# Kernel tuning notes

Measured on AMD Instinct MI355X. Metric: run time of the kernel, lower is better.

The kernel has to match this reference:

```python
import jax, jax.numpy as jnp
import numpy as np

U = 512  # units

def hard_sigmoid(x):
    # Keras hard_sigmoid: clip(0.2*x + 0.5, 0, 1)
    return jnp.clip(0.2 * x + 0.5, 0.0, 1.0)

def setup_inputs() -> dict:
    key = jax.random.key(0)
    ks = jax.random.split(key, 9)
    B, T, A, D = 64, 2048, 512, 512  # batch, annotation steps, annotation units, input dim
    s = lambda k, shape, scale: jax.random.normal(k, shape, jnp.float32) * scale
    return {
        "inputs": s(ks[0], (B, D), 1.0),
        "h": s(ks[1], (B, U), 1.0),
        "c": s(ks[2], (B, U), 1.0),
        "annotations": s(ks[3], (B, T, A), 1.0),
        "kernel": s(ks[4], (D + A, 4 * U), 0.02),
        "recurrent_kernel": s(ks[5], (U, 4 * U), 0.02),
        "bias": jnp.zeros((6 * U,), jnp.float32).at[U:2 * U].set(1.0),  # unit_forget_bias
        "kernel_u": s(ks[6], (A, U), 0.02),
        "kernel_w": s(ks[7], (U, U), 0.02),
        "kernel_v": s(ks[8], (U,), 0.02),
    }

def reference(inputs, h, c, annotations, kernel, recurrent_kernel, bias, kernel_u, kernel_w, kernel_v):
    bias_u = bias[4 * U:5 * U]
    # precomputed annotation projection (done once in build()): [B,T,U]
    uh = jnp.einsum('bta,au->btu', annotations, kernel_u) + bias_u
    # Bahdanau attention scores
    Wxstm = h @ kernel_w                                   # [B,U]
    et = jnp.einsum('btu,u->bt', jnp.tanh(uh + Wxstm[:, None, :]), kernel_v)
    at = jax.nn.softmax(et, axis=1)                        # exp/sum in source == softmax
    context = jnp.einsum('bt,bta->ba', at, annotations)    # [B,A]
    x = jnp.concatenate([inputs, context], axis=-1)        # [B, D+A]
    z = x @ kernel + h @ recurrent_kernel + bias[:4 * U]   # [B,4U]
    i = hard_sigmoid(z[:, :U])
    f = hard_sigmoid(z[:, U:2 * U])
    c_new = f * c + i * jnp.tanh(z[:, 2 * U:3 * U])
    o = hard_sigmoid(z[:, 3 * U:])
    h_new = o * jnp.tanh(c_new)
    return h_new
```

## Files before the change

kernel.cpp:

```cpp
#include <hip/hip_runtime.h>

constexpr int U = 512;
constexpr int B = 64;
constexpr int T = 2048;
constexpr int A = 512;

typedef __attribute__((ext_vector_type(8))) short short8;
typedef __attribute__((ext_vector_type(4))) float f32x4;

__device__ __forceinline__ unsigned short f32_to_bf16(float f) {
    unsigned int b = __float_as_uint(f);
    unsigned int r = (b + 0x7FFFu + ((b >> 16) & 1u)) >> 16;
    return (unsigned short)r;
}

__device__ __forceinline__ float fast_tanh(float x) {
    float e = exp2f(x * 2.885390081777927f);
    return (e - 1.0f) * __builtin_amdgcn_rcpf(e + 1.0f);
}

__device__ __forceinline__ float hard_sigmoid(float z) {
    return fminf(fmaxf(0.2f * z + 0.5f, 0.0f), 1.0f);
}

__global__ __launch_bounds__(256) void k_prep_s(const float* __restrict__ h,
                                                const float* __restrict__ kw,
                                                float* __restrict__ Sp) {
    int b = blockIdx.x >> 2;
    int kc = blockIdx.x & 3;
    int u = threadIdx.x;
    const float* hb = h + b * U + kc * 128;
    const float* kwb = kw + (size_t)kc * 128 * U;
    float a0 = 0.f, a1 = 0.f;
#pragma unroll 4
    for (int k = 0; k < 128; ++k) {
        float hv = hb[k];
        a0 += hv * kwb[(size_t)k * U + u];
        a1 += hv * kwb[(size_t)k * U + u + 256];
    }
    float* p = Sp + ((size_t)kc * 64 + b) * U;
    p[u] = a0;
    p[u + 256] = a1;
}

__global__ __launch_bounds__(256) void k_s_reduce(const float* __restrict__ Sp,
                                                  const float* __restrict__ bias,
                                                  float* __restrict__ S) {
    int gid = blockIdx.x * 256 + threadIdx.x;
    int b = gid >> 9, u = gid & 511;
    float s = bias[4 * U + u];
#pragma unroll
    for (int kc = 0; kc < 4; ++kc) s += Sp[((size_t)kc * 64 + b) * U + u];
    S[gid] = s;
}

__global__ __launch_bounds__(256) void k_prep_kut(const float* __restrict__ ku,
                                                  unsigned short* __restrict__ kut) {
    __shared__ float tile[32][33];
    int a0 = (blockIdx.x >> 4) << 5;
    int u0 = (blockIdx.x & 15) << 5;
    int c = threadIdx.x & 31, r0 = threadIdx.x >> 5;
#pragma unroll
    for (int p = 0; p < 4; ++p) {
        int r = r0 + p * 8;
        tile[r][c] = ku[(a0 + r) * U + u0 + c];
    }
    __syncthreads();
#pragma unroll
    for (int p = 0; p < 4; ++p) {
        int r = r0 + p * 8;
        kut[(u0 + r) * A + a0 + c] = f32_to_bf16(tile[c][r]);
    }
}

__global__ __launch_bounds__(256) void k_prep_wt(const float* __restrict__ kern,
                                                 const float* __restrict__ rk,
                                                 unsigned short* __restrict__ Wt) {
    __shared__ float tile[32][33];
    int k0 = blockIdx.x << 5;
    int j0 = blockIdx.y << 5;
    int c = threadIdx.x & 31, r0 = threadIdx.x >> 5;
#pragma unroll
    for (int p = 0; p < 4; ++p) {
        int r = r0 + p * 8;
        int k = k0 + r;
        float val = (k < 1024) ? kern[k * 2048 + j0 + c]
                               : rk[(k - 1024) * 2048 + j0 + c];
        tile[r][c] = val;
    }
    __syncthreads();
#pragma unroll
    for (int p = 0; p < 4; ++p) {
        int r = r0 + p * 8;
        Wt[(size_t)(j0 + r) * 1536 + k0 + c] = f32_to_bf16(tile[c][r]);
    }
}

__global__ __launch_bounds__(256) void k_gemm_et(const float* __restrict__ ann,
                                                 const unsigned short* __restrict__ kut,
                                                 const float* __restrict__ S,
                                                 const float* __restrict__ v,
                                                 float* __restrict__ etp) {
    __shared__ unsigned short As[128 * 88];
    __shared__ unsigned short Bs[128 * 64];
    __shared__ float red[4][64];

    const int tid = threadIdx.x;
    const int wave = tid >> 6;
    const int lane = tid & 63;
    const int lanelo = lane & 15;
    const int quad = lane >> 4;
    const int wm = wave >> 1, wn = wave & 1;

    const int mt = blockIdx.x >> 2;
    const int nt = blockIdx.x & 3;
    const int b = mt >> 4;
    const float* aBase = ann + (size_t)mt * 128 * A;
    const unsigned short* bBase = kut + (size_t)nt * 128 * A;

    f32x4 acc[4][4];
#pragma unroll
    for (int i = 0; i < 4; ++i)
#pragma unroll
        for (int j = 0; j < 4; ++j) acc[i][j] = {0.f, 0.f, 0.f, 0.f};

    for (int k0 = 0; k0 < A; k0 += 64) {
#pragma unroll
        for (int p = 0; p < 4; ++p) {
            int flat = p * 4096 + wave * 1024 + lane * 16;
            int nl = flat >> 7;
            int d = ((flat >> 4) & 7) ^ (nl & 7);
            __builtin_amdgcn_global_load_lds(
                (const __attribute__((address_space(1))) void*)(bBase + (size_t)nl * A + k0 + d * 8),
                (__attribute__((address_space(3))) void*)((char*)Bs + p * 4096 + wave * 1024),
                16, 0, 0);
        }
#pragma unroll
        for (int p = 0; p < 4; ++p) {
            int flat8 = p * 256 + tid;
            int row = flat8 >> 3;
            int c8 = flat8 & 7;
            const float* src = aBase + (size_t)row * A + k0 + c8 * 8;
            f32x4 v0 = *(const f32x4*)src;
            f32x4 v1 = *(const f32x4*)(src + 4);
            short8 pk;
            pk[0] = (short)f32_to_bf16(v0.x);
            pk[1] = (short)f32_to_bf16(v0.y);
            pk[2] = (short)f32_to_bf16(v0.z);
            pk[3] = (short)f32_to_bf16(v0.w);
            pk[4] = (short)f32_to_bf16(v1.x);
            pk[5] = (short)f32_to_bf16(v1.y);
            pk[6] = (short)f32_to_bf16(v1.z);
            pk[7] = (short)f32_to_bf16(v1.w);
            *(short8*)&As[row * 88 + c8 * 8] = pk;
        }
        __syncthreads();
#pragma unroll
        for (int s = 0; s < 2; ++s) {
            short8 af[4], bfr[4];
#pragma unroll
            for (int mi = 0; mi < 4; ++mi) {
                int row = wm * 64 + mi * 16 + lanelo;
                af[mi] = *(const short8*)&As[row * 88 + s * 32 + quad * 8];
            }
#pragma unroll
            for (int ni = 0; ni < 4; ++ni) {
                int nl = wn * 64 + ni * 16 + lanelo;
                int ch = (s * 4 + quad) ^ (nl & 7);
                bfr[ni] = *(const short8*)&Bs[nl * 64 + ch * 8];
            }
#pragma unroll
            for (int mi = 0; mi < 4; ++mi)
#pragma unroll
                for (int ni = 0; ni < 4; ++ni)
                    acc[mi][ni] = __builtin_amdgcn_mfma_f32_16x16x32_bf16(
                        af[mi], bfr[ni], acc[mi][ni], 0, 0, 0);
        }
        __syncthreads();
    }

    float rows[16];
#pragma unroll
    for (int i = 0; i < 16; ++i) rows[i] = 0.f;
#pragma unroll
    for (int ni = 0; ni < 4; ++ni) {
        int n = nt * 128 + wn * 64 + ni * 16 + lanelo;
        float sv = S[b * U + n];
        float vv = v[n];
#pragma unroll
        for (int mi = 0; mi < 4; ++mi)
#pragma unroll
            for (int r = 0; r < 4; ++r)
                rows[mi * 4 + r] += fast_tanh(acc[mi][ni][r] + sv) * vv;
    }
#pragma unroll
    for (int i = 0; i < 16; ++i) {
        rows[i] += __shfl_xor(rows[i], 1);
        rows[i] += __shfl_xor(rows[i], 2);
        rows[i] += __shfl_xor(rows[i], 4);
        rows[i] += __shfl_xor(rows[i], 8);
    }
    if (lanelo == 0) {
#pragma unroll
        for (int mi = 0; mi < 4; ++mi)
#pragma unroll
            for (int r = 0; r < 4; ++r)
                red[wave][mi * 16 + quad * 4 + r] = rows[mi * 4 + r];
    }
    __syncthreads();
    if (tid < 128) {
        int wmv = tid >> 6, ml = tid & 63;
        float sum = red[wmv * 2][ml] + red[wmv * 2 + 1][ml];
        etp[(size_t)nt * (1024 * 128) + (size_t)mt * 128 + tid] = sum;
    }
}

__global__ __launch_bounds__(256) void k_softmax(const float* __restrict__ etp,
                                                 float* __restrict__ at) {
    __shared__ float sred[256];
    int b = blockIdx.x;
    const float* e = etp + b * T;
    float vals[8];
    float mx = -1e30f;
#pragma unroll
    for (int i = 0; i < 8; ++i) {
        int t = threadIdx.x + i * 256;
        float x = e[t] + e[131072 + t] + e[2 * 131072 + t] + e[3 * 131072 + t];
        vals[i] = x;
        mx = fmaxf(mx, x);
    }
    sred[threadIdx.x] = mx;
    __syncthreads();
    for (int s = 128; s > 0; s >>= 1) {
        if (threadIdx.x < s) sred[threadIdx.x] = fmaxf(sred[threadIdx.x], sred[threadIdx.x + s]);
        __syncthreads();
    }
    mx = sred[0];
    __syncthreads();
    float sum = 0.f;
#pragma unroll
    for (int i = 0; i < 8; ++i) {
        float x = exp2f((vals[i] - mx) * 1.4426950408889634f);
        vals[i] = x;
        sum += x;
    }
    sred[threadIdx.x] = sum;
    __syncthreads();
    for (int s = 128; s > 0; s >>= 1) {
        if (threadIdx.x < s) sred[threadIdx.x] += sred[threadIdx.x + s];
        __syncthreads();
    }
    float inv = 1.0f / sred[0];
#pragma unroll
    for (int i = 0; i < 8; ++i) at[b * T + threadIdx.x + i * 256] = vals[i] * inv;
}

__global__ __launch_bounds__(256) void k_ctx_part(const float* __restrict__ at,
                                                  const float* __restrict__ ann,
                                                  float* __restrict__ part) {
    int b = blockIdx.x >> 4;
    int tc = blockIdx.x & 15;
    int a2 = threadIdx.x << 1;
    const float* annb = ann + ((size_t)b * T + tc * 128) * A;
    const float* atb = at + b * T + tc * 128;
    float acc0 = 0.f, acc1 = 0.f;
    for (int t = 0; t < 128; ++t) {
        float w = atb[t];
        float2 rv = *(const float2*)(annb + (size_t)t * A + a2);
        acc0 += w * rv.x;
        acc1 += w * rv.y;
    }
    float* p = part + ((size_t)b * 16 + tc) * A;
    p[a2] = acc0;
    p[a2 + 1] = acc1;
}

__global__ __launch_bounds__(256) void k_ctx_reduce(const float* __restrict__ part,
                                                    float* __restrict__ ctx) {
    int b = blockIdx.x;
    for (int a = threadIdx.x; a < A; a += 256) {
        float s = 0.f;
#pragma unroll
        for (int c = 0; c < 16; ++c) s += part[((size_t)b * 16 + c) * A + a];
        ctx[b * A + a] = s;
    }
}

__global__ __launch_bounds__(256) void k_prep_xb(const float* __restrict__ inputs,
                                                 const float* __restrict__ ctx,
                                                 const float* __restrict__ h,
                                                 unsigned short* __restrict__ xb) {
    int b = blockIdx.y;
    int k = blockIdx.x * 256 + threadIdx.x;
    float val;
    if (k < 512) val = inputs[b * 512 + k];
    else if (k < 1024) val = ctx[b * 512 + (k - 512)];
    else val = h[b * 512 + (k - 1024)];
    xb[b * 1536 + k] = f32_to_bf16(val);
}

__global__ __launch_bounds__(256) void k_zgemm(const unsigned short* __restrict__ xb,
                                               const unsigned short* __restrict__ Wt,
                                               float* __restrict__ zpart) {
    const int kc = blockIdx.x & 7;
    const int nt = blockIdx.x >> 3;
    const int wave = threadIdx.x >> 6;
    const int lane = threadIdx.x & 63;
    const int lanelo = lane & 15;
    const int quad = lane >> 4;

    const int n = nt * 64 + wave * 16 + lanelo;
    const unsigned short* bp = Wt + (size_t)n * 1536 + kc * 192 + quad * 8;
    const unsigned short* ap = xb + (size_t)lanelo * 1536 + kc * 192 + quad * 8;

    f32x4 acc[4];
#pragma unroll
    for (int i = 0; i < 4; ++i) acc[i] = {0.f, 0.f, 0.f, 0.f};

#pragma unroll
    for (int ks = 0; ks < 6; ++ks) {
        short8 bfrag = *(const short8*)(bp + ks * 32);
#pragma unroll
        for (int mi = 0; mi < 4; ++mi) {
            short8 afrag = *(const short8*)(ap + (size_t)mi * 16 * 1536 + ks * 32);
            acc[mi] = __builtin_amdgcn_mfma_f32_16x16x32_bf16(afrag, bfrag, acc[mi], 0, 0, 0);
        }
    }

    float* p = zpart + (size_t)kc * 64 * 2048;
#pragma unroll
    for (int mi = 0; mi < 4; ++mi)
#pragma unroll
        for (int r = 0; r < 4; ++r) {
            int m = mi * 16 + quad * 4 + r;
            p[(size_t)m * 2048 + n] = acc[mi][r];
        }
}

__global__ __launch_bounds__(256) void k_gates(const float* __restrict__ zpart,
                                               const float* __restrict__ bias,
                                               const float* __restrict__ c,
                                               float* __restrict__ hnew) {
    int gid = blockIdx.x * 256 + threadIdx.x;
    int b = gid >> 9;
    int u = gid & 511;
    float z[4];
#pragma unroll
    for (int g = 0; g < 4; ++g) {
        int j = (g << 9) + u;
        float s = bias[j];
#pragma unroll
        for (int kc = 0; kc < 8; ++kc)
            s += zpart[((size_t)kc * 64 + b) * 2048 + j];
        z[g] = s;
    }
    float ig = hard_sigmoid(z[0]);
    float fg = hard_sigmoid(z[1]);
    float cn = fg * c[b * 512 + u] + ig * fast_tanh(z[2]);
    float og = hard_sigmoid(z[3]);
    hnew[b * 512 + u] = og * fast_tanh(cn);
}

extern "C" void kernel_launch(void* const* d_in, const int* in_sizes, int n_in,
                              void* d_out, int out_size, void* d_ws, size_t ws_size,
                              hipStream_t stream) {
    const float* inputs = (const float*)d_in[0];
    const float* h      = (const float*)d_in[1];
    const float* c      = (const float*)d_in[2];
    const float* ann    = (const float*)d_in[3];
    const float* kern   = (const float*)d_in[4];
    const float* rk     = (const float*)d_in[5];
    const float* bias   = (const float*)d_in[6];
    const float* ku     = (const float*)d_in[7];
    const float* kw     = (const float*)d_in[8];
    const float* kv     = (const float*)d_in[9];

    char* ws = (char*)d_ws;
    float*          S     = (float*)(ws + 0);
    unsigned short* kut   = (unsigned short*)(ws + 131072);
    float*          etp   = (float*)(ws + 655360);
    float*          at    = (float*)(ws + 2752512);
    float*          part  = (float*)(ws + 3276800);
    float*          Sp    = (float*)(ws + 3276800);
    float*          ctx   = (float*)(ws + 5373952);
    unsigned short* xb    = (unsigned short*)(ws + 5505024);
    unsigned short* Wt    = (unsigned short*)(ws + 5701632);
    float*          zpart = (float*)(ws + 11993088);
    float*          hnew  = (float*)d_out;

    k_prep_wt<<<dim3(48, 64), 256, 0, stream>>>(kern, rk, Wt);
    k_prep_kut<<<256, 256, 0, stream>>>(ku, kut);
    k_prep_s<<<256, 256, 0, stream>>>(h, kw, Sp);
    k_s_reduce<<<128, 256, 0, stream>>>(Sp, bias, S);
    k_gemm_et<<<4096, 256, 0, stream>>>(ann, kut, S, kv, etp);
    k_softmax<<<64, 256, 0, stream>>>(etp, at);
    k_ctx_part<<<64 * 16, 256, 0, stream>>>(at, ann, part);
    k_ctx_reduce<<<64, 256, 0, stream>>>(part, ctx);
    k_prep_xb<<<dim3(6, 64), 256, 0, stream>>>(inputs, ctx, h, xb);
    k_zgemm<<<256, 256, 0, stream>>>(xb, Wt, zpart);
    k_gates<<<128, 256, 0, stream>>>(zpart, bias, c, hnew);
}
```

Before: 557.4 us.

## Widen attention-score GEMM N tile to 256 and restructure context partial sums

The score GEMM block tile grows from 128x128 to 128x256, halving the grid so each annotation tile is read from HBM and converted to bf16 only twice instead of four times. The A tile now uses an XOR-swizzled LDS layout instead of padding, and the softmax sums two partial score planes instead of four. The context kernel uses float4 loads with two half-block t-splits reduced in LDS, covering 256 timesteps per block. The wider tile doubles the accumulator registers, which may limit occupancy, so launch bounds request two blocks per SM.

```diff
diff --git a/kernel.cpp b/kernel.cpp
--- a/kernel.cpp
+++ b/kernel.cpp
@@ -96,13 +96,13 @@
     }
 }
 
-__global__ __launch_bounds__(256) void k_gemm_et(const float* __restrict__ ann,
-                                                 const unsigned short* __restrict__ kut,
-                                                 const float* __restrict__ S,
-                                                 const float* __restrict__ v,
-                                                 float* __restrict__ etp) {
-    __shared__ unsigned short As[128 * 88];
-    __shared__ unsigned short Bs[128 * 64];
+__global__ __launch_bounds__(256, 2) void k_gemm_et(const float* __restrict__ ann,
+                                                    const unsigned short* __restrict__ kut,
+                                                    const float* __restrict__ S,
+                                                    const float* __restrict__ v,
+                                                    float* __restrict__ etp) {
+    __shared__ unsigned short As[128 * 64];
+    __shared__ unsigned short Bs[256 * 64];
     __shared__ float red[4][64];
 
     const int tid = threadIdx.x;
@@ -112,27 +112,30 @@
     const int quad = lane >> 4;
     const int wm = wave >> 1, wn = wave & 1;
 
-    const int mt = blockIdx.x >> 2;
-    const int nt = blockIdx.x & 3;
+    const int bid = blockIdx.x;
+    const int nt = (bid >> 3) & 1;
+    const int mt = (bid & 7) | ((bid >> 4) << 3);
     const int b = mt >> 4;
     const float* aBase = ann + (size_t)mt * 128 * A;
-    const unsigned short* bBase = kut + (size_t)nt * 128 * A;
-
-    f32x4 acc[4][4];
+    const unsigned short* bBase = kut + (size_t)nt * 256 * A;
+
+    f32x4 acc[4][8];
 #pragma unroll
     for (int i = 0; i < 4; ++i)
 #pragma unroll
-        for (int j = 0; j < 4; ++j) acc[i][j] = {0.f, 0.f, 0.f, 0.f};
+        for (int j = 0; j < 8; ++j) acc[i][j] = {0.f, 0.f, 0.f, 0.f};
 
     for (int k0 = 0; k0 < A; k0 += 64) {
 #pragma unroll
-        for (int p = 0; p < 4; ++p) {
-            int flat = p * 4096 + wave * 1024 + lane * 16;
-            int nl = flat >> 7;
-            int d = ((flat >> 4) & 7) ^ (nl & 7);
+        for (int p = 0; p < 8; ++p) {
+            int seg = p * 4 + wave;
+            int flat = seg * 1024 + lane * 16;
+            int row = flat >> 7;
+            int sc = (flat >> 4) & 7;
+            int d = sc ^ (row & 7);
             __builtin_amdgcn_global_load_lds(
-                (const __attribute__((address_space(1))) void*)(bBase + (size_t)nl * A + k0 + d * 8),
-                (__attribute__((address_space(3))) void*)((char*)Bs + p * 4096 + wave * 1024),
+                (const __attribute__((address_space(1))) void*)(bBase + (size_t)row * A + k0 + d * 8),
+                (__attribute__((address_space(3))) void*)((char*)Bs + seg * 1024),
                 16, 0, 0);
         }
 #pragma unroll
@@ -152,27 +155,28 @@
             pk[5] = (short)f32_to_bf16(v1.y);
             pk[6] = (short)f32_to_bf16(v1.z);
             pk[7] = (short)f32_to_bf16(v1.w);
-            *(short8*)&As[row * 88 + c8 * 8] = pk;
+            *(short8*)&As[row * 64 + ((c8 ^ (row & 7)) * 8)] = pk;
         }
         __syncthreads();
 #pragma unroll
         for (int s = 0; s < 2; ++s) {
-            short8 af[4], bfr[4];
+            int c = s * 4 + quad;
+            short8 af[4];
 #pragma unroll
             for (int mi = 0; mi < 4; ++mi) {
                 int row = wm * 64 + mi * 16 + lanelo;
-                af[mi] = *(const short8*)&As[row * 88 + s * 32 + quad * 8];
+                af[mi] = *(const short8*)&As[row * 64 + ((c ^ (row & 7)) * 8)];
             }
-#pragma unroll
-            for (int ni = 0; ni < 4; ++ni) {
-                int nl = wn * 64 + ni * 16 + lanelo;
-                int ch = (s * 4 + quad) ^ (nl & 7);
-                bfr[ni] = *(const short8*)&Bs[nl * 64 + ch * 8];
+            short8 bfr[8];
+#pragma unroll
+            for (int ni = 0; ni < 8; ++ni) {
+                int rowb = wn * 128 + ni * 16 + lanelo;
+                bfr[ni] = *(const short8*)&Bs[rowb * 64 + ((c ^ (rowb & 7)) * 8)];
             }
 #pragma unroll
             for (int mi = 0; mi < 4; ++mi)
 #pragma unroll
-                for (int ni = 0; ni < 4; ++ni)
+                for (int ni = 0; ni < 8; ++ni)
                     acc[mi][ni] = __builtin_amdgcn_mfma_f32_16x16x32_bf16(
                         af[mi], bfr[ni], acc[mi][ni], 0, 0, 0);
         }
@@ -183,8 +187,8 @@
 #pragma unroll
     for (int i = 0; i < 16; ++i) rows[i] = 0.f;
 #pragma unroll
-    for (int ni = 0; ni < 4; ++ni) {
-        int n = nt * 128 + wn * 64 + ni * 16 + lanelo;
+    for (int ni = 0; ni < 8; ++ni) {
+        int n = nt * 256 + wn * 128 + ni * 16 + lanelo;
         float sv = S[b * U + n];
         float vv = v[n];
 #pragma unroll
@@ -225,7 +229,7 @@
 #pragma unroll
     for (int i = 0; i < 8; ++i) {
         int t = threadIdx.x + i * 256;
-        float x = e[t] + e[131072 + t] + e[2 * 131072 + t] + e[3 * 131072 + t];
+        float x = e[t] + e[131072 + t];
         vals[i] = x;
         mx = fmaxf(mx, x);
     }
@@ -258,21 +262,30 @@
 __global__ __launch_bounds__(256) void k_ctx_part(const float* __restrict__ at,
                                                   const float* __restrict__ ann,
                                                   float* __restrict__ part) {
-    int b = blockIdx.x >> 4;
-    int tc = blockIdx.x & 15;
+    __shared__ float buf[2][512];
+    int b = blockIdx.x >> 3;
+    int tc = blockIdx.x & 7;
+    int half = threadIdx.x >> 7;
+    int a4 = (threadIdx.x & 127) << 2;
+    const float* annb = ann + ((size_t)b * T + tc * 256) * A;
+    const float* atb = at + b * T + tc * 256;
+    f32x4 acc = {0.f, 0.f, 0.f, 0.f};
+    for (int t = half; t < 256; t += 2) {
+        float w = atb[t];
+        f32x4 rv = *(const f32x4*)(annb + (size_t)t * A + a4);
+        acc.x += w * rv.x;
+        acc.y += w * rv.y;
+        acc.z += w * rv.z;
+        acc.w += w * rv.w;
+    }
+    *(f32x4*)&buf[half][a4] = acc;
+    __syncthreads();
     int a2 = threadIdx.x << 1;
-    const float* annb = ann + ((size_t)b * T + tc * 128) * A;
-    const float* atb = at + b * T + tc * 128;
-    float acc0 = 0.f, acc1 = 0.f;
-    for (int t = 0; t < 128; ++t) {
-        float w = atb[t];
-        float2 rv = *(const float2*)(annb + (size_t)t * A + a2);
-        acc0 += w * rv.x;
-        acc1 += w * rv.y;
-    }
-    float* p = part + ((size_t)b * 16 + tc) * A;
-    p[a2] = acc0;
-    p[a2 + 1] = acc1;
+    float s0 = buf[0][a2] + buf[1][a2];
+    float s1 = buf[0][a2 + 1] + buf[1][a2 + 1];
+    float* p = part + ((size_t)b * 8 + tc) * A;
+    p[a2] = s0;
+    p[a2 + 1] = s1;
 }
 
 __global__ __launch_bounds__(256) void k_ctx_reduce(const float* __restrict__ part,
@@ -281,7 +294,7 @@
     for (int a = threadIdx.x; a < A; a += 256) {
         float s = 0.f;
 #pragma unroll
-        for (int c = 0; c < 16; ++c) s += part[((size_t)b * 16 + c) * A + a];
+        for (int c = 0; c < 8; ++c) s += part[((size_t)b * 8 + c) * A + a];
         ctx[b * A + a] = s;
     }
 }
@@ -379,22 +392,22 @@
     float*          S     = (float*)(ws + 0);
     unsigned short* kut   = (unsigned short*)(ws + 131072);
     float*          etp   = (float*)(ws + 655360);
-    float*          at    = (float*)(ws + 2752512);
-    float*          part  = (float*)(ws + 3276800);
-    float*          Sp    = (float*)(ws + 3276800);
-    float*          ctx   = (float*)(ws + 5373952);
-    unsigned short* xb    = (unsigned short*)(ws + 5505024);
-    unsigned short* Wt    = (unsigned short*)(ws + 5701632);
-    float*          zpart = (float*)(ws + 11993088);
+    float*          at    = (float*)(ws + 1703936);
+    float*          part  = (float*)(ws + 2228224);
+    float*          Sp    = (float*)(ws + 2228224);
+    float*          ctx   = (float*)(ws + 3276800);
+    unsigned short* xb    = (unsigned short*)(ws + 3407872);
+    unsigned short* Wt    = (unsigned short*)(ws + 3604480);
+    float*          zpart = (float*)(ws + 9895936);
     float*          hnew  = (float*)d_out;
 
     k_prep_wt<<<dim3(48, 64), 256, 0, stream>>>(kern, rk, Wt);
     k_prep_kut<<<256, 256, 0, stream>>>(ku, kut);
     k_prep_s<<<256, 256, 0, stream>>>(h, kw, Sp);
     k_s_reduce<<<128, 256, 0, stream>>>(Sp, bias, S);
-    k_gemm_et<<<4096, 256, 0, stream>>>(ann, kut, S, kv, etp);
+    k_gemm_et<<<2048, 256, 0, stream>>>(ann, kut, S, kv, etp);
     k_softmax<<<64, 256, 0, stream>>>(etp, at);
-    k_ctx_part<<<64 * 16, 256, 0, stream>>>(at, ann, part);
+    k_ctx_part<<<64 * 8, 256, 0, stream>>>(at, ann, part);
     k_ctx_reduce<<<64, 256, 0, stream>>>(part, ctx);
     k_prep_xb<<<dim3(6, 64), 256, 0, stream>>>(inputs, ctx, h, xb);
     k_zgemm<<<256, 256, 0, stream>>>(xb, Wt, zpart);
```

Result: faster. 516.7 us (-7.3%).
